# Kernel optimization log

Measured on AMD Instinct MI355X. Metric: run time of the kernel, lower is better.

The kernel has to match this reference:

```python
import jax, jax.numpy as jnp
import numpy as np

N, F_IN, HID, E, G = 100000, 256, 256, 800000, 256


def setup_inputs() -> dict:
    key = jax.random.key(0)
    ks = jax.random.split(key, 10)
    x = jax.random.normal(ks[0], (N, F_IN), dtype=jnp.float32)
    edge_index = jax.random.randint(ks[1], (2, E), 0, N, dtype=jnp.int64)
    batch = jnp.sort(jax.random.randint(ks[2], (N,), 0, G, dtype=jnp.int64))
    s = 1.0 / np.sqrt(HID)
    W1 = jax.random.normal(ks[3], (F_IN, HID), dtype=jnp.float32) * s
    b1 = jnp.zeros((HID,), dtype=jnp.float32)
    W2 = jax.random.normal(ks[4], (HID, HID), dtype=jnp.float32) * s
    b2 = jnp.zeros((HID,), dtype=jnp.float32)
    Wc1 = jax.random.normal(ks[5], (HID, HID // 2), dtype=jnp.float32) * s
    bc1 = jnp.zeros((HID // 2,), dtype=jnp.float32)
    Wc2 = jax.random.normal(ks[6], (HID // 2, 2), dtype=jnp.float32) * s
    bc2 = jnp.zeros((2,), dtype=jnp.float32)
    return dict(x=x, edge_index=edge_index, batch=batch, num_graphs=G,
                W1=W1, b1=b1, W2=W2, b2=b2, Wc1=Wc1, bc1=bc1, Wc2=Wc2, bc2=bc2)


def _gcn_layer(h, src, dst, inv_sqrt_deg, W, b):
    # GCNConv: D^-1/2 (A + I) D^-1/2 (h W) + b
    hw = h @ W                                            # (N, H)
    coef = inv_sqrt_deg[src] * inv_sqrt_deg[dst]          # (E,)
    msgs = hw[src] * coef[:, None]                        # (E, H)
    agg = jax.ops.segment_sum(msgs, dst, num_segments=h.shape[0])
    self_loop = hw * (inv_sqrt_deg * inv_sqrt_deg)[:, None]
    return agg + self_loop + b


def reference(x, edge_index, batch, num_graphs, W1, b1, W2, b2, Wc1, bc1, Wc2, bc2):
    n = x.shape[0]
    src, dst = edge_index[0], edge_index[1]
    # degree with self-loops (symmetric normalization)
    deg = jax.ops.segment_sum(jnp.ones((src.shape[0],), jnp.float32), dst,
                              num_segments=n) + 1.0
    inv_sqrt_deg = jax.lax.rsqrt(deg)

    h = jax.nn.relu(_gcn_layer(x, src, dst, inv_sqrt_deg, W1, b1))
    node_emb = jax.nn.relu(_gcn_layer(h, src, dst, inv_sqrt_deg, W2, b2))

    # per-graph mean pooling (segment mean replacing the Python loop)
    sums = jax.ops.segment_sum(node_emb, batch, num_segments=num_graphs)
    counts = jax.ops.segment_sum(jnp.ones((n,), jnp.float32), batch,
                                 num_segments=num_graphs)
    graph_emb = sums / jnp.maximum(counts, 1.0)[:, None]

    # classifier MLP (dropout is identity in eval mode)
    hcls = jax.nn.relu(graph_emb @ Wc1 + bc1)
    logits = hcls @ Wc2 + bc2                             # (G, 2)
    return logits, node_emb
```

## Files before the change

### kernel.cpp

```cpp
#include <hip/hip_runtime.h>
#include <hip/hip_bf16.h>

#define HID 256
#define NGRAPH 256

typedef __bf16 bf16_t;
typedef __attribute__((ext_vector_type(8))) __bf16 bf16x8;
typedef __attribute__((ext_vector_type(4))) __bf16 bf16x4;
typedef __attribute__((ext_vector_type(4))) float f32x4;

__global__ void zero_int_kernel(int* __restrict__ p, int n) {
    int i = blockIdx.x * blockDim.x + threadIdx.x;
    if (i < n) p[i] = 0;
}

__global__ void count_deg_kernel(const int* __restrict__ ei, int E, int* __restrict__ deg) {
    int e = blockIdx.x * blockDim.x + threadIdx.x;
    if (e >= E) return;
    int dst = ei[E + e];
    atomicAdd(&deg[dst], 1);
}

#define SCHUNK 512

__global__ __launch_bounds__(256) void scan_pass1_kernel(
    const int* __restrict__ deg, int N, int* __restrict__ bsum) {
    __shared__ int red[256];
    int b = blockIdx.x, t = threadIdx.x;
    int i0 = b * SCHUNK + 2 * t;
    int v = 0;
    if (i0 < N) v += deg[i0];
    if (i0 + 1 < N) v += deg[i0 + 1];
    red[t] = v;
    __syncthreads();
    for (int s = 128; s > 0; s >>= 1) {
        if (t < s) red[t] += red[t + s];
        __syncthreads();
    }
    if (t == 0) bsum[b] = red[0];
}

__global__ __launch_bounds__(256) void scan_pass2_kernel(
    const int* __restrict__ bsum, int NB, int* __restrict__ boff) {
    __shared__ int s[256];
    int t = threadIdx.x;
    int v = (t < NB) ? bsum[t] : 0;
    s[t] = v;
    __syncthreads();
    for (int off = 1; off < 256; off <<= 1) {
        int x = s[t];
        if (t >= off) x += s[t - off];
        __syncthreads();
        s[t] = x;
        __syncthreads();
    }
    if (t < NB) boff[t] = s[t] - v;
}

__global__ __launch_bounds__(256) void scan_pass3_kernel(
    const int* __restrict__ deg, int N, const int* __restrict__ boff,
    int* __restrict__ rowptr, int* __restrict__ cursor, float* __restrict__ invd) {
    __shared__ int s[256];
    int b = blockIdx.x, t = threadIdx.x;
    int i0 = b * SCHUNK + 2 * t;
    int d0 = (i0 < N) ? deg[i0] : 0;
    int d1 = (i0 + 1 < N) ? deg[i0 + 1] : 0;
    int pair = d0 + d1;
    s[t] = pair;
    __syncthreads();
    for (int off = 1; off < 256; off <<= 1) {
        int x = s[t];
        if (t >= off) x += s[t - off];
        __syncthreads();
        s[t] = x;
        __syncthreads();
    }
    int excl = s[t] - pair + boff[b];
    if (i0 < N) {
        rowptr[i0] = excl;
        cursor[i0] = excl;
        invd[i0] = rsqrtf((float)d0 + 1.0f);
    }
    if (i0 + 1 < N) {
        int e1 = excl + d0;
        rowptr[i0 + 1] = e1;
        cursor[i0 + 1] = e1;
        invd[i0 + 1] = rsqrtf((float)d1 + 1.0f);
    }
}

__global__ void fill_csr_kernel(const int* __restrict__ ei, int E,
                                int* __restrict__ cursor, int* __restrict__ csr_src) {
    int e = blockIdx.x * blockDim.x + threadIdx.x;
    if (e >= E) return;
    int src = ei[e];
    int dst = ei[E + e];
    int pos = atomicAdd(&cursor[dst], 1);
    csr_src[pos] = src;
}

__global__ __launch_bounds__(256) void wsplit_kernel(
    const float* __restrict__ W, bf16_t* __restrict__ Wf) {
    int idx = blockIdx.x * 256 + threadIdx.x;
    float w = W[idx];
    int k = idx >> 8, n = idx & 255;
    int k0 = k >> 5, kg = (k >> 3) & 3, j = k & 7;
    int nt = n >> 4, m = n & 15;
    Wf[(size_t)(((k0 * 16 + nt) * 64) + kg * 16 + m) * 8 + j] = (bf16_t)w;
}

#define GBM 64

template <int SPLIT>
__global__ __launch_bounds__(256, 2) void gemm_mfma_kernel(
    const void* __restrict__ Xv, const bf16_t* __restrict__ Wf,
    const float* __restrict__ rowscale, bf16_t* __restrict__ out, int Nrows) {
    const int tid = threadIdx.x;
    const int wave = tid >> 6;
    const int lane = tid & 63;
    const int row0 = blockIdx.x * GBM;
    const int m = lane & 15;
    const int kg = lane >> 4;

    const int arow_raw = row0 + wave * 16 + m;
    const int arow = (arow_raw < Nrows) ? arow_raw : 0;

    f32x4 acc[16];
#pragma unroll
    for (int i = 0; i < 16; ++i) acc[i] = (f32x4){0.f, 0.f, 0.f, 0.f};

#pragma unroll
    for (int k0 = 0; k0 < 8; ++k0) {
        bf16x8 ah, al;
        if (SPLIT) {
            const float* xrow = (const float*)Xv + (size_t)arow * 256 + kg * 8;
            float4 xa = *(const float4*)&xrow[k0 * 32];
            float4 xb = *(const float4*)&xrow[k0 * 32 + 4];
            float xf[8] = {xa.x, xa.y, xa.z, xa.w, xb.x, xb.y, xb.z, xb.w};
#pragma unroll
            for (int q = 0; q < 8; ++q) {
                bf16_t hi = (bf16_t)xf[q];
                ah[q] = hi;
                al[q] = (bf16_t)(xf[q] - (float)hi);
            }
        } else {
            const bf16_t* xrow = (const bf16_t*)Xv + (size_t)arow * 256 + kg * 8;
            ah = *(const bf16x8*)&xrow[k0 * 32];
        }
        const bf16_t* wfk = Wf + (size_t)(k0 * 16) * 64 * 8 + (size_t)lane * 8;
        bf16x8 bh[16];
#pragma unroll
        for (int nt = 0; nt < 16; ++nt)
            bh[nt] = *(const bf16x8*)(wfk + (size_t)nt * 64 * 8);
#pragma unroll
        for (int nt = 0; nt < 16; ++nt) {
            acc[nt] = __builtin_amdgcn_mfma_f32_16x16x32_bf16(ah, bh[nt], acc[nt], 0, 0, 0);
            if (SPLIT)
                acc[nt] = __builtin_amdgcn_mfma_f32_16x16x32_bf16(al, bh[nt], acc[nt], 0, 0, 0);
        }
    }

    const int rbase = row0 + wave * 16 + kg * 4;
#pragma unroll
    for (int j = 0; j < 4; ++j) {
        int r = rbase + j;
        if (r < Nrows) {
            float sc = rowscale[r];
#pragma unroll
            for (int nt = 0; nt < 16; ++nt)
                out[(size_t)r * 256 + nt * 16 + m] = (bf16_t)(acc[nt][j] * sc);
        }
    }
}

template <typename OutT>
__global__ __launch_bounds__(256) void gcn_aggregate_kernel(
    const bf16_t* __restrict__ hs, const int* __restrict__ rowptr,
    const int* __restrict__ deg, const int* __restrict__ csr_src,
    const float* __restrict__ inv_d, const float* __restrict__ bias,
    OutT* __restrict__ out, int N) {
    int gwid = (blockIdx.x * blockDim.x + threadIdx.x) >> 6;
    int lane = threadIdx.x & 63;
    if (gwid >= N) return;
    int base = rowptr[gwid];
    int len = deg[gwid];
    int c = lane * 4;

    bf16x4 sv = *(const bf16x4*)&hs[(size_t)gwid * 256 + c];
    float ax0 = (float)sv[0], ay0 = (float)sv[1], az0 = (float)sv[2], aw0 = (float)sv[3];
    float ax1 = 0.f, ay1 = 0.f, az1 = 0.f, aw1 = 0.f;
    float ax2 = 0.f, ay2 = 0.f, az2 = 0.f, aw2 = 0.f;
    float ax3 = 0.f, ay3 = 0.f, az3 = 0.f, aw3 = 0.f;
    int i = 0;
    for (; i + 4 <= len; i += 4) {
        int s0 = csr_src[base + i];
        int s1 = csr_src[base + i + 1];
        int s2 = csr_src[base + i + 2];
        int s3 = csr_src[base + i + 3];
        bf16x4 v0 = *(const bf16x4*)&hs[(size_t)s0 * 256 + c];
        bf16x4 v1 = *(const bf16x4*)&hs[(size_t)s1 * 256 + c];
        bf16x4 v2 = *(const bf16x4*)&hs[(size_t)s2 * 256 + c];
        bf16x4 v3 = *(const bf16x4*)&hs[(size_t)s3 * 256 + c];
        ax0 += (float)v0[0]; ay0 += (float)v0[1]; az0 += (float)v0[2]; aw0 += (float)v0[3];
        ax1 += (float)v1[0]; ay1 += (float)v1[1]; az1 += (float)v1[2]; aw1 += (float)v1[3];
        ax2 += (float)v2[0]; ay2 += (float)v2[1]; az2 += (float)v2[2]; aw2 += (float)v2[3];
        ax3 += (float)v3[0]; ay3 += (float)v3[1]; az3 += (float)v3[2]; aw3 += (float)v3[3];
    }
    for (; i < len; ++i) {
        int s = csr_src[base + i];
        bf16x4 v = *(const bf16x4*)&hs[(size_t)s * 256 + c];
        ax0 += (float)v[0]; ay0 += (float)v[1]; az0 += (float)v[2]; aw0 += (float)v[3];
    }
    float ax = (ax0 + ax1) + (ax2 + ax3);
    float ay = (ay0 + ay1) + (ay2 + ay3);
    float az = (az0 + az1) + (az2 + az3);
    float aw = (aw0 + aw1) + (aw2 + aw3);

    float sc = inv_d[gwid];
    float4 bb = *(const float4*)&bias[c];
    float ox = fmaxf(fmaf(ax, sc, bb.x), 0.f);
    float oy = fmaxf(fmaf(ay, sc, bb.y), 0.f);
    float oz = fmaxf(fmaf(az, sc, bb.z), 0.f);
    float ow = fmaxf(fmaf(aw, sc, bb.w), 0.f);
    if constexpr (sizeof(OutT) == 2) {
        bf16x4 o;
        o[0] = (bf16_t)ox; o[1] = (bf16_t)oy; o[2] = (bf16_t)oz; o[3] = (bf16_t)ow;
        *(bf16x4*)&out[(size_t)gwid * 256 + c] = o;
    } else {
        float4 o = {ox, oy, oz, ow};
        *(float4*)&out[(size_t)gwid * 256 + c] = o;
    }
}

__global__ void graph_bounds_kernel(const int* __restrict__ batch, int N, int G,
                                    int* __restrict__ gstart) {
    int i = blockIdx.x * blockDim.x + threadIdx.x;
    if (i > N) return;
    int cur = (i < N) ? batch[i] : G;
    int prev = (i == 0) ? -1 : batch[i - 1];
    for (int g = prev + 1; g <= cur; ++g) gstart[g] = i;
}

__global__ __launch_bounds__(256) void pool_mean_kernel(
    const float* __restrict__ emb, const int* __restrict__ gstart,
    float* __restrict__ gemb) {
    int g = blockIdx.x;
    int j = threadIdx.x;
    int s = gstart[g], e = gstart[g + 1];
    float s0 = 0.f, s1 = 0.f, s2 = 0.f, s3 = 0.f;
    int n = s;
    for (; n + 4 <= e; n += 4) {
        s0 += emb[(size_t)n * 256 + j];
        s1 += emb[(size_t)(n + 1) * 256 + j];
        s2 += emb[(size_t)(n + 2) * 256 + j];
        s3 += emb[(size_t)(n + 3) * 256 + j];
    }
    for (; n < e; ++n) s0 += emb[(size_t)n * 256 + j];
    float sum = (s0 + s1) + (s2 + s3);
    float cnt = fmaxf((float)(e - s), 1.0f);
    gemb[g * 256 + j] = sum / cnt;
}

__global__ __launch_bounds__(128) void cls1_kernel(
    const float* __restrict__ gemb, const float* __restrict__ Wc1,
    const float* __restrict__ bc1, float* __restrict__ hcls) {
    int g = blockIdx.x;
    int j = threadIdx.x;
    float sum = bc1[j];
    for (int k = 0; k < 256; ++k) sum = fmaf(gemb[g * 256 + k], Wc1[k * 128 + j], sum);
    hcls[g * 128 + j] = fmaxf(sum, 0.f);
}

__global__ void cls2_kernel(const float* __restrict__ hcls, const float* __restrict__ Wc2,
                            const float* __restrict__ bc2, float* __restrict__ logits, int G) {
    int idx = blockIdx.x * blockDim.x + threadIdx.x;
    if (idx >= G * 2) return;
    int g = idx >> 1, c = idx & 1;
    float sum = bc2[c];
    for (int k = 0; k < 128; ++k) sum = fmaf(hcls[g * 128 + k], Wc2[k * 2 + c], sum);
    logits[idx] = sum;
}

extern "C" void kernel_launch(void* const* d_in, const int* in_sizes, int n_in,
                              void* d_out, int out_size, void* d_ws, size_t ws_size,
                              hipStream_t stream) {
    const float* x   = (const float*)d_in[0];
    const int*   ei  = (const int*)d_in[1];
    const int*   batch = (const int*)d_in[2];
    const float* W1  = (const float*)d_in[4];
    const float* b1  = (const float*)d_in[5];
    const float* W2  = (const float*)d_in[6];
    const float* b2  = (const float*)d_in[7];
    const float* Wc1 = (const float*)d_in[8];
    const float* bc1 = (const float*)d_in[9];
    const float* Wc2 = (const float*)d_in[10];
    const float* bc2 = (const float*)d_in[11];

    const int N = in_sizes[0] / HID;
    const int E = in_sizes[1] / 2;
    const int G = NGRAPH;

    float* logits   = (float*)d_out;
    float* node_out = (float*)d_out + (size_t)G * 2;

    char* wsb = (char*)d_ws;
    size_t off = 0;
    auto alloc = [&](size_t bytes) -> void* {
        void* p = wsb + off;
        off += (bytes + 255) & ~(size_t)255;
        return p;
    };
    bf16_t* hs     = (bf16_t*)alloc((size_t)N * HID * 2);
    bf16_t* hb     = (bf16_t*)alloc((size_t)N * HID * 2);
    int*    rowptr = (int*)alloc((size_t)N * 4);
    int*    cursor = (int*)alloc((size_t)N * 4);
    int*    degi   = (int*)alloc((size_t)N * 4);
    int*    csr    = (int*)alloc((size_t)E * 4);
    float*  invd   = (float*)alloc((size_t)N * 4);
    int*    gstart = (int*)alloc((size_t)(G + 1) * 4);
    float*  gemb   = (float*)alloc((size_t)G * HID * 4);
    float*  hcls   = (float*)alloc((size_t)G * (HID / 2) * 4);
    int*    bsum   = (int*)alloc(256 * 4);
    int*    boff   = (int*)alloc(256 * 4);
    bf16_t* wf     = (bf16_t*)alloc((size_t)HID * HID * 2);
    (void)ws_size; (void)n_in; (void)out_size;

    const int NB = (N + SCHUNK - 1) / SCHUNK;

    zero_int_kernel<<<(N + 255) / 256, 256, 0, stream>>>(degi, N);
    count_deg_kernel<<<(E + 255) / 256, 256, 0, stream>>>(ei, E, degi);
    scan_pass1_kernel<<<NB, 256, 0, stream>>>(degi, N, bsum);
    scan_pass2_kernel<<<1, 256, 0, stream>>>(bsum, NB, boff);
    scan_pass3_kernel<<<NB, 256, 0, stream>>>(degi, N, boff, rowptr, cursor, invd);
    fill_csr_kernel<<<(E + 255) / 256, 256, 0, stream>>>(ei, E, cursor, csr);

    const int GB = (N + GBM - 1) / GBM;

    wsplit_kernel<<<HID * HID / 256, 256, 0, stream>>>(W1, wf);
    gemm_mfma_kernel<1><<<GB, 256, 0, stream>>>(x, wf, invd, hs, N);
    gcn_aggregate_kernel<bf16_t><<<(N * 64 + 255) / 256, 256, 0, stream>>>(
        hs, rowptr, degi, csr, invd, b1, hb, N);

    wsplit_kernel<<<HID * HID / 256, 256, 0, stream>>>(W2, wf);
    gemm_mfma_kernel<0><<<GB, 256, 0, stream>>>(hb, wf, invd, hs, N);
    gcn_aggregate_kernel<float><<<(N * 64 + 255) / 256, 256, 0, stream>>>(
        hs, rowptr, degi, csr, invd, b2, node_out, N);

    graph_bounds_kernel<<<(N + 1 + 255) / 256, 256, 0, stream>>>(batch, N, G, gstart);
    pool_mean_kernel<<<G, 256, 0, stream>>>(node_out, gstart, gemb);
    cls1_kernel<<<G, 128, 0, stream>>>(gemb, Wc1, bc1, hcls);
    cls2_kernel<<<(G * 2 + 255) / 256, 256, 0, stream>>>(hcls, Wc2, bc2, logits, G);
}
```

Baseline: 428.4 us.

## Stage weight fragments in LDS and batch activation loads per K-half

The MFMA GEMM now copies each half of the pre-swizzled bf16 weight matrix (64 KB) into shared memory cooperatively and has every wave read B fragments from LDS. Before, each wave fetched them directly from global memory. It also issues all four activation loads for a K-half up front so their latency overlaps with the weight staging. The goal is to cut redundant global/L2 traffic for W across the four waves. The cost is two barriers per block and 64 KB of LDS per block, which limits occupancy to about two blocks per CU.

```diff
diff --git a/kernel.cpp b/kernel.cpp
--- a/kernel.cpp
+++ b/kernel.cpp
@@ -115,6 +115,8 @@
 __global__ __launch_bounds__(256, 2) void gemm_mfma_kernel(
     const void* __restrict__ Xv, const bf16_t* __restrict__ Wf,
     const float* __restrict__ rowscale, bf16_t* __restrict__ out, int Nrows) {
+    __shared__ bf16_t Blds[32768];
+
     const int tid = threadIdx.x;
     const int wave = tid >> 6;
     const int lane = tid & 63;
@@ -130,33 +132,56 @@
     for (int i = 0; i < 16; ++i) acc[i] = (f32x4){0.f, 0.f, 0.f, 0.f};
 
 #pragma unroll
-    for (int k0 = 0; k0 < 8; ++k0) {
-        bf16x8 ah, al;
+    for (int c = 0; c < 2; ++c) {
+        float4 xa0, xb0, xa1, xb1, xa2, xb2, xa3, xb3;
+        bf16x8 ah0, ah1, ah2, ah3;
         if (SPLIT) {
-            const float* xrow = (const float*)Xv + (size_t)arow * 256 + kg * 8;
-            float4 xa = *(const float4*)&xrow[k0 * 32];
-            float4 xb = *(const float4*)&xrow[k0 * 32 + 4];
-            float xf[8] = {xa.x, xa.y, xa.z, xa.w, xb.x, xb.y, xb.z, xb.w};
-#pragma unroll
-            for (int q = 0; q < 8; ++q) {
-                bf16_t hi = (bf16_t)xf[q];
-                ah[q] = hi;
-                al[q] = (bf16_t)(xf[q] - (float)hi);
+            const float* xr = (const float*)Xv + (size_t)arow * 256 + c * 128 + kg * 8;
+            xa0 = *(const float4*)&xr[0];   xb0 = *(const float4*)&xr[4];
+            xa1 = *(const float4*)&xr[32];  xb1 = *(const float4*)&xr[36];
+            xa2 = *(const float4*)&xr[64];  xb2 = *(const float4*)&xr[68];
+            xa3 = *(const float4*)&xr[96];  xb3 = *(const float4*)&xr[100];
+        } else {
+            const bf16_t* xr = (const bf16_t*)Xv + (size_t)arow * 256 + c * 128 + kg * 8;
+            ah0 = *(const bf16x8*)&xr[0];
+            ah1 = *(const bf16x8*)&xr[32];
+            ah2 = *(const bf16x8*)&xr[64];
+            ah3 = *(const bf16x8*)&xr[96];
+        }
+
+        if (c) __syncthreads();
+#pragma unroll
+        for (int it = 0; it < 16; ++it)
+            *(bf16x8*)&Blds[it * 2048 + tid * 8] =
+                *(const bf16x8*)&Wf[c * 32768 + it * 2048 + tid * 8];
+        __syncthreads();
+
+#pragma unroll
+        for (int k0c = 0; k0c < 4; ++k0c) {
+            bf16x8 ah, al;
+            if (SPLIT) {
+                float4 xa = (k0c == 0) ? xa0 : (k0c == 1) ? xa1 : (k0c == 2) ? xa2 : xa3;
+                float4 xb = (k0c == 0) ? xb0 : (k0c == 1) ? xb1 : (k0c == 2) ? xb2 : xb3;
+                float xf[8] = {xa.x, xa.y, xa.z, xa.w, xb.x, xb.y, xb.z, xb.w};
+#pragma unroll
+                for (int q = 0; q < 8; ++q) {
+                    bf16_t hi = (bf16_t)xf[q];
+                    ah[q] = hi;
+                    al[q] = (bf16_t)(xf[q] - (float)hi);
+                }
+            } else {
+                ah = (k0c == 0) ? ah0 : (k0c == 1) ? ah1 : (k0c == 2) ? ah2 : ah3;
             }
-        } else {
-            const bf16_t* xrow = (const bf16_t*)Xv + (size_t)arow * 256 + kg * 8;
-            ah = *(const bf16x8*)&xrow[k0 * 32];
-        }
-        const bf16_t* wfk = Wf + (size_t)(k0 * 16) * 64 * 8 + (size_t)lane * 8;
-        bf16x8 bh[16];
-#pragma unroll
-        for (int nt = 0; nt < 16; ++nt)
-            bh[nt] = *(const bf16x8*)(wfk + (size_t)nt * 64 * 8);
-#pragma unroll
-        for (int nt = 0; nt < 16; ++nt) {
-            acc[nt] = __builtin_amdgcn_mfma_f32_16x16x32_bf16(ah, bh[nt], acc[nt], 0, 0, 0);
-            if (SPLIT)
-                acc[nt] = __builtin_amdgcn_mfma_f32_16x16x32_bf16(al, bh[nt], acc[nt], 0, 0, 0);
+            bf16x8 bh[16];
+#pragma unroll
+            for (int nt = 0; nt < 16; ++nt)
+                bh[nt] = *(const bf16x8*)&Blds[(k0c * 16 + nt) * 512 + lane * 8];
+#pragma unroll
+            for (int nt = 0; nt < 16; ++nt) {
+                acc[nt] = __builtin_amdgcn_mfma_f32_16x16x32_bf16(ah, bh[nt], acc[nt], 0, 0, 0);
+                if (SPLIT)
+                    acc[nt] = __builtin_amdgcn_mfma_f32_16x16x32_bf16(al, bh[nt], acc[nt], 0, 0, 0);
+            }
         }
     }
 
```

Result: faster. 383.0 us (-10.6%).
